# Performance work log

Hardware: AMD Instinct MI355X
Metric: run time of the kernel (lower is better)

## Reference

```python
import jax, jax.numpy as jnp
import numpy as np

IN_DIM = 1024
CTX_DIM = 768
NUM_HEADS = 16
HEAD_DIM = IN_DIM // NUM_HEADS
SCALE = 1.0 / float(np.sqrt(HEAD_DIM))


def setup_inputs() -> dict:
    key = jax.random.key(0)
    ks = jax.random.split(key, 10)
    B, NQ, NKV = 8, 1024, 512
    s_in = 1.0 / float(np.sqrt(IN_DIM))
    s_ctx = 1.0 / float(np.sqrt(CTX_DIM))
    return {
        "x": jax.random.normal(ks[0], (B, NQ, IN_DIM), dtype=jnp.float32),
        "context": jax.random.normal(ks[1], (B, NKV, CTX_DIM), dtype=jnp.float32),
        "Wq": jax.random.normal(ks[2], (IN_DIM, IN_DIM), dtype=jnp.float32) * s_in,
        "bq": jax.random.normal(ks[3], (IN_DIM,), dtype=jnp.float32) * 0.01,
        "Wk": jax.random.normal(ks[4], (IN_DIM, CTX_DIM), dtype=jnp.float32) * s_ctx,
        "bk": jax.random.normal(ks[5], (IN_DIM,), dtype=jnp.float32) * 0.01,
        "Wv": jax.random.normal(ks[6], (IN_DIM, CTX_DIM), dtype=jnp.float32) * s_ctx,
        "bv": jax.random.normal(ks[7], (IN_DIM,), dtype=jnp.float32) * 0.01,
        "Wo": jax.random.normal(ks[8], (IN_DIM, IN_DIM), dtype=jnp.float32) * s_in,
        "bo": jax.random.normal(ks[9], (IN_DIM,), dtype=jnp.float32) * 0.01,
    }


def reference(x, context, Wq, bq, Wk, bk, Wv, bv, Wo, bo):
    # Linear projections (torch Linear: y = x @ W.T + b)
    q = x @ Wq.T + bq              # [B, Nq, in_dim]
    k = context @ Wk.T + bk        # [B, Nkv, in_dim]
    v = context @ Wv.T + bv        # [B, Nkv, in_dim]
    B, NQ, _ = q.shape
    NKV = k.shape[1]
    q = q.reshape(B, NQ, NUM_HEADS, HEAD_DIM)
    k = k.reshape(B, NKV, NUM_HEADS, HEAD_DIM)
    v = v.reshape(B, NKV, NUM_HEADS, HEAD_DIM)
    attn = jnp.einsum('bihd,bjhd->bhij', q, k) * SCALE   # [B, H, Nq, Nkv]
    # the half-batch split in the original is mathematically identical to
    # a plain softmax over the last dim
    attn = jax.nn.softmax(attn, axis=-1)
    out = jnp.einsum('bhij,bjhd->bihd', attn, v)          # [B, Nq, H, Dh]
    out = out.reshape(B, NQ, IN_DIM)
    return out @ Wo.T + bo
```

## Files before the change

### kernel.cpp

```cpp
#include <hip/hip_runtime.h>
#include <math.h>

#define IN_DIM    1024
#define CTX_DIM   768
#define NUM_HEADS 16
#define HEAD_DIM  64
#define BATCH     8
#define NQ        1024
#define NKV       512
#define C2LOG     0.18033688f

typedef __attribute__((ext_vector_type(8)))  _Float16 f16x8;
typedef __attribute__((ext_vector_type(4)))  _Float16 f16x4;
typedef __attribute__((ext_vector_type(2)))  _Float16 f16x2;
typedef __attribute__((ext_vector_type(4)))  float    f32x4;
typedef __attribute__((ext_vector_type(16))) float    f32x16;

__device__ __forceinline__ void async16(const void* g, void* l) {
    __builtin_amdgcn_global_load_lds(
        (const __attribute__((address_space(1))) void*)g,
        (__attribute__((address_space(3))) void*)l, 16, 0, 0);
}

__device__ __forceinline__ float fexp2(float x) {
    float r; asm("v_exp_f32 %0, %1" : "=v"(r) : "v"(x)); return r;
}

__device__ __forceinline__ void plswap(int& a, int& b) {
    asm volatile("v_permlane32_swap_b32 %0, %1" : "+v"(a), "+v"(b));
}

__global__ __launch_bounds__(256)
void cvt6(const float* __restrict__ s0, const float* __restrict__ s1,
          const float* __restrict__ s2, const float* __restrict__ s3,
          const float* __restrict__ s4, const float* __restrict__ s5,
          _Float16* __restrict__ dst)
{
    const int stride = gridDim.x * blockDim.x;
    for (int i = blockIdx.x * blockDim.x + threadIdx.x; i < 3801088; i += stride) {
        const float* s; int loc;
        if      (i < 2097152) { s = s0; loc = i; }
        else if (i < 2883584) { s = s1; loc = i - 2097152; }
        else if (i < 3145728) { s = s2; loc = i - 2883584; }
        else if (i < 3342336) { s = s3; loc = i - 3145728; }
        else if (i < 3538944) { s = s4; loc = i - 3342336; }
        else                  { s = s5; loc = i - 3538944; }
        float4 v = *(const float4*)(s + (size_t)loc * 4);
        f16x4 o;
        o.x = (_Float16)v.x; o.y = (_Float16)v.y;
        o.z = (_Float16)v.z; o.w = (_Float16)v.w;
        *(f16x4*)(dst + (size_t)i * 4) = o;
    }
}

template<int BN, int NN, bool TRV, typename OutT>
__global__ __launch_bounds__(256)
void gemm_h(const _Float16* __restrict__ A,
            const _Float16* __restrict__ W0, const float* __restrict__ bias0, OutT* __restrict__ C0,
            const _Float16* __restrict__ W1, const float* __restrict__ bias1, OutT* __restrict__ C1,
            int M, int N, int K)
{
    constexpr int BM = 128, BK = 64;
    constexpr int NF = BN / 32;
    constexpr int CL = BN + 8;
    __shared__ alignas(16) union {
        struct { _Float16 A[2][BM * BK]; _Float16 W[2][BN * BK]; } st;
        _Float16 ce[BM * CL];
    } lds;

    const _Float16* W   = blockIdx.y ? W1 : W0;
    const float*   bias = blockIdx.y ? bias1 : bias0;
    OutT*          C    = blockIdx.y ? C1 : C0;

    const int tid = threadIdx.x;
    const int l   = tid & 63;
    const int w   = tid >> 6;
    const int wr  = w >> 1, wc = w & 1;

    const int per  = gridDim.x >> 3;
    const int tile = (blockIdx.x & 7) * per + (blockIdx.x >> 3);
    const int m0   = (tile / NN) * BM;
    const int n0   = (tile % NN) * BN;

    int aOff[2][4], bOff[2][NF];
    #pragma unroll
    for (int kk = 0; kk < 2; ++kk) {
        #pragma unroll
        for (int m = 0; m < 4; ++m) {
            int rr = wr * 64 + m * 16 + (l & 15);
            aOff[kk][m] = rr * 64 + (((kk * 4 + (l >> 4)) ^ (rr & 7)) * 8);
        }
        #pragma unroll
        for (int n = 0; n < NF; ++n) {
            int rr = wc * (BN / 2) + n * 16 + (l & 15);
            bOff[kk][n] = rr * 64 + (((kk * 4 + (l >> 4)) ^ (rr & 7)) * 8);
        }
    }

    f32x4 acc[4][NF];
    #pragma unroll
    for (int m = 0; m < 4; ++m)
        #pragma unroll
        for (int n = 0; n < NF; ++n)
            acc[m][n] = (f32x4){0.f, 0.f, 0.f, 0.f};

#define GSTAGE(buf, k0) do {                                                    \
        _Pragma("unroll")                                                       \
        for (int it_ = 0; it_ < 4; ++it_) {                                     \
            int e = it_ * 256 + tid, r = e >> 3, p = e & 7;                     \
            async16(A + (size_t)(m0 + r) * K + (k0) + ((p ^ (r & 7)) * 8),      \
                    &lds.st.A[buf][(it_ * 256 + (tid & ~63)) * 8]);             \
        }                                                                       \
        _Pragma("unroll")                                                       \
        for (int it_ = 0; it_ < BN / 32; ++it_) {                               \
            int e = it_ * 256 + tid, r = e >> 3, p = e & 7;                     \
            async16(W + (size_t)(n0 + r) * K + (k0) + ((p ^ (r & 7)) * 8),      \
                    &lds.st.W[buf][(it_ * 256 + (tid & ~63)) * 8]);             \
        }                                                                       \
    } while (0)

    const int nk = K / BK;
    GSTAGE(0, 0);
    __syncthreads();

    for (int kt = 0; kt < nk; ++kt) {
        const int cur = kt & 1;
        if (kt + 1 < nk) GSTAGE(cur ^ 1, (kt + 1) * BK);

        const _Float16* As = lds.st.A[cur];
        const _Float16* Ws = lds.st.W[cur];
        #pragma unroll
        for (int kk = 0; kk < 2; ++kk) {
            f16x8 af[4], bf[NF];
            #pragma unroll
            for (int m = 0; m < 4; ++m) af[m] = *(const f16x8*)&As[aOff[kk][m]];
            #pragma unroll
            for (int n = 0; n < NF; ++n) bf[n] = *(const f16x8*)&Ws[bOff[kk][n]];
            #pragma unroll
            for (int m = 0; m < 4; ++m)
                #pragma unroll
                for (int n = 0; n < NF; ++n)
                    acc[m][n] = __builtin_amdgcn_mfma_f32_16x16x32_f16(
                        af[m], bf[n], acc[m][n], 0, 0, 0);
        }
        __syncthreads();
    }
#undef GSTAGE

    float bv[NF];
    #pragma unroll
    for (int n = 0; n < NF; ++n)
        bv[n] = bias[n0 + wc * (BN / 2) + n * 16 + (l & 15)];

    if constexpr (sizeof(OutT) == 2) {
        #pragma unroll
        for (int m = 0; m < 4; ++m)
            #pragma unroll
            for (int n = 0; n < NF; ++n)
                #pragma unroll
                for (int r = 0; r < 4; ++r) {
                    int row = wr * 64 + m * 16 + (l >> 4) * 4 + r;
                    int col = wc * (BN / 2) + n * 16 + (l & 15);
                    lds.ce[row * CL + col] = (_Float16)(acc[m][n][r] + bv[n]);
                }
        __syncthreads();
        bool trv = TRV && (blockIdx.y == 1);
        if (TRV && trv) {
            const int bb = m0 >> 9, kv0 = m0 & 511, hh = n0 >> 6;
            for (int i = tid; i < 64 * 16; i += 256) {
                int d = i & 63, c = i >> 6;
                f16x8 v;
                #pragma unroll
                for (int j = 0; j < 8; ++j) v[j] = lds.ce[(c * 8 + j) * CL + d];
                *(f16x8*)((_Float16*)C + ((size_t)(bb * 16 + hh) * 64 + d) * NKV
                                       + kv0 + c * 8) = v;
            }
        } else {
            constexpr int SPR = BN / 8;
            for (int i = tid; i < BM * SPR; i += 256) {
                int r = i / SPR, s = i % SPR;
                *(f16x8*)((_Float16*)C + (size_t)(m0 + r) * N + n0 + s * 8) =
                    *(const f16x8*)&lds.ce[r * CL + s * 8];
            }
        }
    } else {
        #pragma unroll
        for (int m = 0; m < 4; ++m)
            #pragma unroll
            for (int n = 0; n < NF; ++n)
                #pragma unroll
                for (int r = 0; r < 4; ++r) {
                    int row = m0 + wr * 64 + m * 16 + (l >> 4) * 4 + r;
                    int col = n0 + wc * (BN / 2) + n * 16 + (l & 15);
                    C[(size_t)row * N + col] = (OutT)(acc[m][n][r] + bv[n]);
                }
    }
}

__global__ __launch_bounds__(256)
void attn_mfma(const _Float16* __restrict__ Qh, const _Float16* __restrict__ Kh,
               const _Float16* __restrict__ Vt, _Float16* __restrict__ Ah)
{
    __shared__ alignas(16) union {
        struct { _Float16 K[2][64 * 64]; _Float16 V[2][64 * 64]; } st;
        _Float16 ot[4][32 * 72];
    } lds;

    const int tid = threadIdx.x;
    const int l = tid & 63, w = tid >> 6;
    const int hi = l >> 5, ln = l & 31;
    const int t  = ((int)blockIdx.x & 7) * 128 + ((int)blockIdx.x >> 3);
    const int qt = t & 7, h = (t >> 3) & 15, b = t >> 7;
    const int q0 = qt * 128;

    f16x8 qa[4];
    {
        const _Float16* qp = Qh + ((size_t)(b * NQ) + q0 + w * 32 + ln) * IN_DIM
                                + h * 64 + hi * 8;
        #pragma unroll
        for (int ks = 0; ks < 4; ++ks) qa[ks] = *(const f16x8*)(qp + ks * 16);
        #pragma unroll
        for (int ks = 0; ks < 4; ++ks)
            #pragma unroll
            for (int j = 0; j < 8; ++j) qa[ks][j] *= (_Float16)C2LOG;
    }

    const _Float16* Kbase = Kh + (size_t)(b * NKV) * IN_DIM + h * 64;
    const _Float16* Vbase = Vt + ((size_t)(b * 16 + h) * 64) * NKV;

#define STAGE(buf, kv0) do {                                                     \
        _Pragma("unroll")                                                        \
        for (int it_ = 0; it_ < 2; ++it_) {                                      \
            int e = it_ * 256 + tid, r = e >> 3, p = e & 7;                      \
            async16(Kbase + (size_t)((kv0) + r) * IN_DIM + ((p ^ (r & 7)) * 8),  \
                    &lds.st.K[buf][(it_ * 256 + (tid & ~63)) * 8]);              \
        }                                                                        \
        _Pragma("unroll")                                                        \
        for (int it_ = 0; it_ < 2; ++it_) {                                      \
            int e = it_ * 256 + tid, r = e >> 3, p = e & 7;                      \
            async16(Vbase + (size_t)r * NKV + (kv0) + ((p ^ (r & 7)) * 8),       \
                    &lds.st.V[buf][(it_ * 256 + (tid & ~63)) * 8]);              \
        }                                                                        \
    } while (0)

    f32x16 oacc[2];
    #pragma unroll
    for (int dt = 0; dt < 2; ++dt)
        #pragma unroll
        for (int i = 0; i < 16; ++i) oacc[dt][i] = 0.f;
    float m2 = -1e30f, lr = 0.f;

    STAGE(0, 0);
    __syncthreads();

    for (int kt = 0; kt < NKV / 64; ++kt) {
        const int cur = kt & 1;
        if (kt < NKV / 64 - 1) STAGE(cur ^ 1, (kt + 1) * 64);

        f32x16 sf[2];
        #pragma unroll
        for (int st = 0; st < 2; ++st)
            #pragma unroll
            for (int i = 0; i < 16; ++i) sf[st][i] = 0.f;

        __builtin_amdgcn_s_setprio(1);
        #pragma unroll
        for (int st = 0; st < 2; ++st) {
            int kvr = st * 32 + ln;
            #pragma unroll
            for (int ks = 0; ks < 4; ++ks) {
                f16x8 kf = *(const f16x8*)
                    &lds.st.K[cur][kvr * 64 + (((ks * 2 + hi) ^ (kvr & 7)) * 8)];
                sf[st] = __builtin_amdgcn_mfma_f32_32x32x16_f16(kf, qa[ks], sf[st], 0, 0, 0);
            }
        }
        __builtin_amdgcn_s_setprio(0);

        float t0[16];
        #pragma unroll
        for (int i = 0; i < 16; ++i) t0[i] = fmaxf(sf[0][i], sf[1][i]);
        #pragma unroll
        for (int s = 8; s; s >>= 1)
            #pragma unroll
            for (int i = 0; i < s; ++i) t0[i] = fmaxf(t0[i], t0[i + s]);
        float pmax = fmaxf(t0[0], __shfl_xor(t0[0], 32));

        if (__any((int)(pmax > m2 + 8.f))) {
            float mn = fmaxf(m2, pmax);
            float corr = fexp2(m2 - mn);
            lr *= corr; m2 = mn;
            #pragma unroll
            for (int dt = 0; dt < 2; ++dt)
                #pragma unroll
                for (int i = 0; i < 16; ++i) oacc[dt][i] *= corr;
        }

        #pragma unroll
        for (int st = 0; st < 2; ++st)
            #pragma unroll
            for (int i = 0; i < 16; ++i) sf[st][i] = fexp2(sf[st][i] - m2);

        #pragma unroll
        for (int i = 0; i < 16; ++i) t0[i] = sf[0][i] + sf[1][i];
        #pragma unroll
        for (int s = 8; s; s >>= 1)
            #pragma unroll
            for (int i = 0; i < s; ++i) t0[i] += t0[i + s];
        lr += t0[0] + __shfl_xor(t0[0], 32);

        int wds[2][8];
        #pragma unroll
        for (int st = 0; st < 2; ++st)
            #pragma unroll
            for (int i = 0; i < 8; ++i) {
                f16x2 p2; p2.x = (_Float16)sf[st][2 * i]; p2.y = (_Float16)sf[st][2 * i + 1];
                wds[st][i] = __builtin_bit_cast(int, p2);
            }
        #pragma unroll
        for (int st = 0; st < 2; ++st) {
            plswap(wds[st][0], wds[st][2]);
            plswap(wds[st][1], wds[st][3]);
            plswap(wds[st][4], wds[st][6]);
            plswap(wds[st][5], wds[st][7]);
        }

        __builtin_amdgcn_s_setprio(1);
        #pragma unroll
        for (int st = 0; st < 2; ++st)
            #pragma unroll
            for (int ks2 = 0; ks2 < 2; ++ks2) {
                union { int i[4]; f16x8 v; } pu;
                #pragma unroll
                for (int k = 0; k < 4; ++k) pu.i[k] = wds[st][ks2 * 4 + k];
                #pragma unroll
                for (int dt = 0; dt < 2; ++dt) {
                    int dr = dt * 32 + ln;
                    f16x8 vf = *(const f16x8*)
                        &lds.st.V[cur][dr * 64 + (((st * 4 + ks2 * 2 + hi) ^ (dr & 7)) * 8)];
                    oacc[dt] = __builtin_amdgcn_mfma_f32_32x32x16_f16(vf, pu.v, oacc[dt], 0, 0, 0);
                }
            }
        __builtin_amdgcn_s_setprio(0);
        __syncthreads();
    }
#undef STAGE

    __syncthreads();
    float inv = 1.f / lr;
    #pragma unroll
    for (int dt = 0; dt < 2; ++dt)
        #pragma unroll
        for (int rq = 0; rq < 4; ++rq) {
            f16x4 v;
            #pragma unroll
            for (int k = 0; k < 4; ++k)
                v[k] = (_Float16)(oacc[dt][rq * 4 + k] * inv);
            int d0 = dt * 32 + rq * 8 + hi * 4;
            *(f16x4*)&lds.ot[w][ln * 72 + d0] = v;
        }
    __syncthreads();
    #pragma unroll
    for (int it = 0; it < 4; ++it) {
        int i = it * 256 + tid;
        int q = i >> 3, s = i & 7;
        f16x8 v = *(const f16x8*)&lds.ot[q >> 5][(q & 31) * 72 + s * 8];
        *(f16x8*)(Ah + ((size_t)(b * NQ) + q0 + q) * IN_DIM + h * 64 + s * 8) = v;
    }
}

extern "C" void kernel_launch(void* const* d_in, const int* in_sizes, int n_in,
                              void* d_out, int out_size, void* d_ws, size_t ws_size,
                              hipStream_t stream)
{
    const float* x   = (const float*)d_in[0];
    const float* ctx = (const float*)d_in[1];
    const float* Wq  = (const float*)d_in[2];
    const float* bq  = (const float*)d_in[3];
    const float* Wk  = (const float*)d_in[4];
    const float* bk  = (const float*)d_in[5];
    const float* Wv  = (const float*)d_in[6];
    const float* bv  = (const float*)d_in[7];
    const float* Wo  = (const float*)d_in[8];
    const float* bo  = (const float*)d_in[9];
    float* out = (float*)d_out;

    _Float16* H = (_Float16*)d_ws;
    _Float16* xh   = H +        0;
    _Float16* ctxh = H +  8388608;
    _Float16* wqh  = H + 11534336;
    _Float16* wkh  = H + 12582912;
    _Float16* wvh  = H + 13369344;
    _Float16* woh  = H + 14155776;
    _Float16* Qh   = H + 15204352;
    _Float16* Kh   = H + 23592960;
    _Float16* Vth  = H + 31981568;
    _Float16* Ah   = H + 36175872;

    const int MQ = BATCH * NQ;
    const int MK = BATCH * NKV;

    cvt6<<<2048, 256, 0, stream>>>(x, ctx, Wq, Wk, Wv, Wo, xh);

    gemm_h<128, 8, false, _Float16><<<dim3(512, 1), 256, 0, stream>>>(
        xh, wqh, bq, Qh, wqh, bq, Qh, MQ, IN_DIM, IN_DIM);
    gemm_h<64, 16, true, _Float16><<<dim3(512, 2), 256, 0, stream>>>(
        ctxh, wkh, bk, Kh, wvh, bv, Vth, MK, IN_DIM, CTX_DIM);

    attn_mfma<<<1024, 256, 0, stream>>>(Qh, Kh, Vth, Ah);

    gemm_h<128, 8, false, float><<<dim3(512, 1), 256, 0, stream>>>(
        Ah, woh, bo, out, woh, bo, out, MQ, IN_DIM, IN_DIM);
}
```

Baseline: 208.4 us.

## Merge Q/K/V projections into one launch and fold softmax scale into Wq

Combines the Q projection and the K/V projection GEMMs into a single 1024-block kernel that dispatches on tile index, with K/V now using 128-wide N tiles. The softmax scale (times log2 e) is folded into the fp16 Wq conversion and the Q bias, which removes the per-thread Q scaling in the attention kernel. The output projection gets its own specialised kernel, and a redundant barrier before the attention epilogue is dropped. This saves one launch and lets Q and K/V blocks share the GPU, at the cost of more branchy setup. Pre-scaling in fp16 changes rounding of Q slightly.

```diff
diff --git a/kernel.cpp b/kernel.cpp
--- a/kernel.cpp
+++ b/kernel.cpp
@@ -1,5 +1,4 @@
 #include <hip/hip_runtime.h>
-#include <math.h>
 
 #define IN_DIM    1024
 #define CTX_DIM   768
@@ -45,44 +44,47 @@
         else if (i < 3342336) { s = s3; loc = i - 3145728; }
         else if (i < 3538944) { s = s4; loc = i - 3342336; }
         else                  { s = s5; loc = i - 3538944; }
+        float sc = (i >= 2883584 && i < 3145728) ? C2LOG : 1.0f;
         float4 v = *(const float4*)(s + (size_t)loc * 4);
         f16x4 o;
-        o.x = (_Float16)v.x; o.y = (_Float16)v.y;
-        o.z = (_Float16)v.z; o.w = (_Float16)v.w;
+        o.x = (_Float16)(v.x * sc); o.y = (_Float16)(v.y * sc);
+        o.z = (_Float16)(v.z * sc); o.w = (_Float16)(v.w * sc);
         *(f16x4*)(dst + (size_t)i * 4) = o;
     }
 }
 
-template<int BN, int NN, bool TRV, typename OutT>
 __global__ __launch_bounds__(256)
-void gemm_h(const _Float16* __restrict__ A,
-            const _Float16* __restrict__ W0, const float* __restrict__ bias0, OutT* __restrict__ C0,
-            const _Float16* __restrict__ W1, const float* __restrict__ bias1, OutT* __restrict__ C1,
-            int M, int N, int K)
+void proj_qkv(const _Float16* __restrict__ xh, const _Float16* __restrict__ ctxh,
+              const _Float16* __restrict__ wqh, const float* __restrict__ bq,
+              const _Float16* __restrict__ wkh, const float* __restrict__ bk,
+              const _Float16* __restrict__ wvh, const float* __restrict__ bv,
+              _Float16* __restrict__ Qh, _Float16* __restrict__ Kh,
+              _Float16* __restrict__ Vth)
 {
-    constexpr int BM = 128, BK = 64;
-    constexpr int NF = BN / 32;
-    constexpr int CL = BN + 8;
+    constexpr int BK = 64, CL = 136;
     __shared__ alignas(16) union {
-        struct { _Float16 A[2][BM * BK]; _Float16 W[2][BN * BK]; } st;
-        _Float16 ce[BM * CL];
+        struct { _Float16 A[2][128 * BK]; _Float16 W[2][128 * BK]; } st;
+        _Float16 ce[128 * CL];
     } lds;
-
-    const _Float16* W   = blockIdx.y ? W1 : W0;
-    const float*   bias = blockIdx.y ? bias1 : bias0;
-    OutT*          C    = blockIdx.y ? C1 : C0;
 
     const int tid = threadIdx.x;
     const int l   = tid & 63;
     const int w   = tid >> 6;
     const int wr  = w >> 1, wc = w & 1;
 
-    const int per  = gridDim.x >> 3;
-    const int tile = (blockIdx.x & 7) * per + (blockIdx.x >> 3);
-    const int m0   = (tile / NN) * BM;
-    const int n0   = (tile % NN) * BN;
-
-    int aOff[2][4], bOff[2][NF];
+    const int tile = ((int)blockIdx.x & 7) * 128 + ((int)blockIdx.x >> 3);
+    const _Float16* A; const _Float16* W; const float* bias; _Float16* C;
+    int K, m0, n0, mode;
+    if (tile < 512)      { mode = 0; A = xh;   W = wqh; bias = bq; C = Qh; K = 1024;
+                           m0 = (tile >> 3) * 128;        n0 = (tile & 7) * 128; }
+    else if (tile < 768) { int s = tile - 512; mode = 1; A = ctxh; W = wkh; bias = bk;
+                           C = Kh; K = 768;
+                           m0 = (s >> 3) * 128;           n0 = (s & 7) * 128; }
+    else                 { int s = tile - 768; mode = 2; A = ctxh; W = wvh; bias = bv;
+                           C = Vth; K = 768;
+                           m0 = (s >> 3) * 128;           n0 = (s & 7) * 128; }
+
+    int aOff[2][4], bOff[2][4];
     #pragma unroll
     for (int kk = 0; kk < 2; ++kk) {
         #pragma unroll
@@ -91,17 +93,17 @@
             aOff[kk][m] = rr * 64 + (((kk * 4 + (l >> 4)) ^ (rr & 7)) * 8);
         }
         #pragma unroll
-        for (int n = 0; n < NF; ++n) {
-            int rr = wc * (BN / 2) + n * 16 + (l & 15);
+        for (int n = 0; n < 4; ++n) {
+            int rr = wc * 64 + n * 16 + (l & 15);
             bOff[kk][n] = rr * 64 + (((kk * 4 + (l >> 4)) ^ (rr & 7)) * 8);
         }
     }
 
-    f32x4 acc[4][NF];
+    f32x4 acc[4][4];
     #pragma unroll
     for (int m = 0; m < 4; ++m)
         #pragma unroll
-        for (int n = 0; n < NF; ++n)
+        for (int n = 0; n < 4; ++n)
             acc[m][n] = (f32x4){0.f, 0.f, 0.f, 0.f};
 
 #define GSTAGE(buf, k0) do {                                                    \
@@ -112,7 +114,7 @@
                     &lds.st.A[buf][(it_ * 256 + (tid & ~63)) * 8]);             \
         }                                                                       \
         _Pragma("unroll")                                                       \
-        for (int it_ = 0; it_ < BN / 32; ++it_) {                               \
+        for (int it_ = 0; it_ < 4; ++it_) {                                     \
             int e = it_ * 256 + tid, r = e >> 3, p = e & 7;                     \
             async16(W + (size_t)(n0 + r) * K + (k0) + ((p ^ (r & 7)) * 8),      \
                     &lds.st.W[buf][(it_ * 256 + (tid & ~63)) * 8]);             \
@@ -131,15 +133,15 @@
         const _Float16* Ws = lds.st.W[cur];
         #pragma unroll
         for (int kk = 0; kk < 2; ++kk) {
-            f16x8 af[4], bf[NF];
+            f16x8 af[4], bf[4];
             #pragma unroll
             for (int m = 0; m < 4; ++m) af[m] = *(const f16x8*)&As[aOff[kk][m]];
             #pragma unroll
-            for (int n = 0; n < NF; ++n) bf[n] = *(const f16x8*)&Ws[bOff[kk][n]];
+            for (int n = 0; n < 4; ++n) bf[n] = *(const f16x8*)&Ws[bOff[kk][n]];
             #pragma unroll
             for (int m = 0; m < 4; ++m)
                 #pragma unroll
-                for (int n = 0; n < NF; ++n)
+                for (int n = 0; n < 4; ++n)
                     acc[m][n] = __builtin_amdgcn_mfma_f32_16x16x32_f16(
                         af[m], bf[n], acc[m][n], 0, 0, 0);
         }
@@ -147,54 +149,142 @@
     }
 #undef GSTAGE
 
-    float bv[NF];
-    #pragma unroll
-    for (int n = 0; n < NF; ++n)
-        bv[n] = bias[n0 + wc * (BN / 2) + n * 16 + (l & 15)];
-
-    if constexpr (sizeof(OutT) == 2) {
-        #pragma unroll
-        for (int m = 0; m < 4; ++m)
-            #pragma unroll
-            for (int n = 0; n < NF; ++n)
+    const float bsc = (mode == 0) ? C2LOG : 1.0f;
+    float bv_[4];
+    #pragma unroll
+    for (int n = 0; n < 4; ++n)
+        bv_[n] = bias[n0 + wc * 64 + n * 16 + (l & 15)] * bsc;
+
+    #pragma unroll
+    for (int m = 0; m < 4; ++m)
+        #pragma unroll
+        for (int n = 0; n < 4; ++n)
+            #pragma unroll
+            for (int r = 0; r < 4; ++r) {
+                int row = wr * 64 + m * 16 + (l >> 4) * 4 + r;
+                int col = wc * 64 + n * 16 + (l & 15);
+                lds.ce[row * CL + col] = (_Float16)(acc[m][n][r] + bv_[n]);
+            }
+    __syncthreads();
+
+    if (mode == 2) {
+        const int bb = m0 >> 9, kv0 = m0 & 511, hh0 = n0 >> 6;
+        #pragma unroll
+        for (int it = 0; it < 8; ++it) {
+            int i = it * 256 + tid;
+            int d = i & 127, c = i >> 7;
+            f16x8 v;
+            #pragma unroll
+            for (int j = 0; j < 8; ++j) v[j] = lds.ce[(c * 8 + j) * CL + d];
+            *(f16x8*)(Vth + ((size_t)(bb * 16 + hh0 + (d >> 6)) * 64 + (d & 63)) * NKV
+                          + kv0 + c * 8) = v;
+        }
+    } else {
+        #pragma unroll
+        for (int it = 0; it < 8; ++it) {
+            int i = it * 256 + tid;
+            int r = i >> 4, s = i & 15;
+            *(f16x8*)(C + (size_t)(m0 + r) * IN_DIM + n0 + s * 8) =
+                *(const f16x8*)&lds.ce[r * CL + s * 8];
+        }
+    }
+}
+
+__global__ __launch_bounds__(256)
+void gemm_out(const _Float16* __restrict__ A, const _Float16* __restrict__ W,
+              const float* __restrict__ bias, float* __restrict__ C)
+{
+    constexpr int BK = 64, K = 1024;
+    __shared__ alignas(16) struct { _Float16 A[2][128 * BK]; _Float16 W[2][128 * BK]; } lds;
+
+    const int tid = threadIdx.x;
+    const int l   = tid & 63;
+    const int w   = tid >> 6;
+    const int wr  = w >> 1, wc = w & 1;
+
+    const int per  = gridDim.x >> 3;
+    const int tile = ((int)blockIdx.x & 7) * per + ((int)blockIdx.x >> 3);
+    const int m0   = (tile >> 3) * 128;
+    const int n0   = (tile & 7) * 128;
+
+    int aOff[2][4], bOff[2][4];
+    #pragma unroll
+    for (int kk = 0; kk < 2; ++kk) {
+        #pragma unroll
+        for (int m = 0; m < 4; ++m) {
+            int rr = wr * 64 + m * 16 + (l & 15);
+            aOff[kk][m] = rr * 64 + (((kk * 4 + (l >> 4)) ^ (rr & 7)) * 8);
+        }
+        #pragma unroll
+        for (int n = 0; n < 4; ++n) {
+            int rr = wc * 64 + n * 16 + (l & 15);
+            bOff[kk][n] = rr * 64 + (((kk * 4 + (l >> 4)) ^ (rr & 7)) * 8);
+        }
+    }
+
+    f32x4 acc[4][4];
+    #pragma unroll
+    for (int m = 0; m < 4; ++m)
+        #pragma unroll
+        for (int n = 0; n < 4; ++n)
+            acc[m][n] = (f32x4){0.f, 0.f, 0.f, 0.f};
+
+#define GSTAGE(buf, k0) do {                                                    \
+        _Pragma("unroll")                                                       \
+        for (int it_ = 0; it_ < 4; ++it_) {                                     \
+            int e = it_ * 256 + tid, r = e >> 3, p = e & 7;                     \
+            async16(A + (size_t)(m0 + r) * K + (k0) + ((p ^ (r & 7)) * 8),      \
+                    &lds.A[buf][(it_ * 256 + (tid & ~63)) * 8]);                \
+        }                                                                       \
+        _Pragma("unroll")                                                       \
+        for (int it_ = 0; it_ < 4; ++it_) {                                     \
+            int e = it_ * 256 + tid, r = e >> 3, p = e & 7;                     \
+            async16(W + (size_t)(n0 + r) * K + (k0) + ((p ^ (r & 7)) * 8),      \
+                    &lds.W[buf][(it_ * 256 + (tid & ~63)) * 8]);                \
+        }                                                                       \
+    } while (0)
+
+    GSTAGE(0, 0);
+    __syncthreads();
+
+    for (int kt = 0; kt < 16; ++kt) {
+        const int cur = kt & 1;
+        if (kt + 1 < 16) GSTAGE(cur ^ 1, (kt + 1) * BK);
+
+        const _Float16* As = lds.A[cur];
+        const _Float16* Ws = lds.W[cur];
+        #pragma unroll
+        for (int kk = 0; kk < 2; ++kk) {
+            f16x8 af[4], bf[4];
+            #pragma unroll
+            for (int m = 0; m < 4; ++m) af[m] = *(const f16x8*)&As[aOff[kk][m]];
+            #pragma unroll
+            for (int n = 0; n < 4; ++n) bf[n] = *(const f16x8*)&Ws[bOff[kk][n]];
+            #pragma unroll
+            for (int m = 0; m < 4; ++m)
                 #pragma unroll
-                for (int r = 0; r < 4; ++r) {
-                    int row = wr * 64 + m * 16 + (l >> 4) * 4 + r;
-                    int col = wc * (BN / 2) + n * 16 + (l & 15);
-                    lds.ce[row * CL + col] = (_Float16)(acc[m][n][r] + bv[n]);
-                }
+                for (int n = 0; n < 4; ++n)
+                    acc[m][n] = __builtin_amdgcn_mfma_f32_16x16x32_f16(
+                        af[m], bf[n], acc[m][n], 0, 0, 0);
+        }
         __syncthreads();
-        bool trv = TRV && (blockIdx.y == 1);
-        if (TRV && trv) {
-            const int bb = m0 >> 9, kv0 = m0 & 511, hh = n0 >> 6;
-            for (int i = tid; i < 64 * 16; i += 256) {
-                int d = i & 63, c = i >> 6;
-                f16x8 v;
-                #pragma unroll
-                for (int j = 0; j < 8; ++j) v[j] = lds.ce[(c * 8 + j) * CL + d];
-                *(f16x8*)((_Float16*)C + ((size_t)(bb * 16 + hh) * 64 + d) * NKV
-                                       + kv0 + c * 8) = v;
+    }
+#undef GSTAGE
+
+    float bv_[4];
+    #pragma unroll
+    for (int n = 0; n < 4; ++n)
+        bv_[n] = bias[n0 + wc * 64 + n * 16 + (l & 15)];
+    #pragma unroll
+    for (int m = 0; m < 4; ++m)
+        #pragma unroll
+        for (int n = 0; n < 4; ++n)
+            #pragma unroll
+            for (int r = 0; r < 4; ++r) {
+                int row = m0 + wr * 64 + m * 16 + (l >> 4) * 4 + r;
+                int col = n0 + wc * 64 + n * 16 + (l & 15);
+                C[(size_t)row * IN_DIM + col] = acc[m][n][r] + bv_[n];
             }
-        } else {
-            constexpr int SPR = BN / 8;
-            for (int i = tid; i < BM * SPR; i += 256) {
-                int r = i / SPR, s = i % SPR;
-                *(f16x8*)((_Float16*)C + (size_t)(m0 + r) * N + n0 + s * 8) =
-                    *(const f16x8*)&lds.ce[r * CL + s * 8];
-            }
-        }
-    } else {
-        #pragma unroll
-        for (int m = 0; m < 4; ++m)
-            #pragma unroll
-            for (int n = 0; n < NF; ++n)
-                #pragma unroll
-                for (int r = 0; r < 4; ++r) {
-                    int row = m0 + wr * 64 + m * 16 + (l >> 4) * 4 + r;
-                    int col = n0 + wc * (BN / 2) + n * 16 + (l & 15);
-                    C[(size_t)row * N + col] = (OutT)(acc[m][n][r] + bv[n]);
-                }
-    }
 }
 
 __global__ __launch_bounds__(256)
@@ -219,10 +309,6 @@
                                 + h * 64 + hi * 8;
         #pragma unroll
         for (int ks = 0; ks < 4; ++ks) qa[ks] = *(const f16x8*)(qp + ks * 16);
-        #pragma unroll
-        for (int ks = 0; ks < 4; ++ks)
-            #pragma unroll
-            for (int j = 0; j < 8; ++j) qa[ks][j] *= (_Float16)C2LOG;
     }
 
     const _Float16* Kbase = Kh + (size_t)(b * NKV) * IN_DIM + h * 64;
@@ -345,7 +431,6 @@
     }
 #undef STAGE
 
-    __syncthreads();
     float inv = 1.f / lr;
     #pragma unroll
     for (int dt = 0; dt < 2; ++dt)
@@ -396,18 +481,12 @@
     _Float16* Vth  = H + 31981568;
     _Float16* Ah   = H + 36175872;
 
-    const int MQ = BATCH * NQ;
-    const int MK = BATCH * NKV;
-
     cvt6<<<2048, 256, 0, stream>>>(x, ctx, Wq, Wk, Wv, Wo, xh);
 
-    gemm_h<128, 8, false, _Float16><<<dim3(512, 1), 256, 0, stream>>>(
-        xh, wqh, bq, Qh, wqh, bq, Qh, MQ, IN_DIM, IN_DIM);
-    gemm_h<64, 16, true, _Float16><<<dim3(512, 2), 256, 0, stream>>>(
-        ctxh, wkh, bk, Kh, wvh, bv, Vth, MK, IN_DIM, CTX_DIM);
+    proj_qkv<<<1024, 256, 0, stream>>>(xh, ctxh, wqh, bq, wkh, bk, wvh, bv,
+                                       Qh, Kh, Vth);
 
     attn_mfma<<<1024, 256, 0, stream>>>(Qh, Kh, Vth, Ah);
 
-    gemm_h<128, 8, false, float><<<dim3(512, 1), 256, 0, stream>>>(
-        Ah, woh, bo, out, woh, bo, out, MQ, IN_DIM, IN_DIM);
-}
+    gemm_out<<<512, 256, 0, stream>>>(Ah, woh, bo, out);
+}
```

Measured after the change: 214.1 us. +2.7%, slower.
